# Kernel tuning notes

Hardware: AMD Instinct MI355X
Metric: run time of the kernel (lower is better)

The kernel has to match this reference:

```python
import jax, jax.numpy as jnp
import numpy as np

S = 1024      # graphs (frames / LSTM seq_len)
NPG = 64      # nodes per graph
N = S * NPG   # total nodes
E = 524288    # total edges (512 per graph)
NF, EF = 32, 16
HC = 64       # hidden_channels
H1 = 3        # gat1 heads
NEG_SLOPE = 0.2


def _p(k, shape):
    return 0.1 * jax.random.normal(k, shape, dtype=jnp.float32)


def setup_inputs():
    key = jax.random.key(0)
    ks = jax.random.split(key, 30)
    x = jax.random.normal(ks[0], (N, NF), jnp.float32)
    local = jax.random.randint(ks[1], (2, E), 0, NPG)
    off = jnp.repeat(jnp.arange(S) * NPG, E // S)  # edges grouped per graph
    edge_index = local + off[None, :]
    edge_attr = jax.random.normal(ks[2], (E, EF), jnp.float32)
    batch = jnp.repeat(jnp.arange(S), NPG)
    return {
        'x': x, 'edge_index': edge_index, 'edge_attr': edge_attr, 'batch': batch,
        # gat1: in=NF, out=HC, heads=H1, edge_dim=EF
        'Wl1': _p(ks[3], (NF, H1 * HC)), 'bl1': _p(ks[4], (H1 * HC,)),
        'Wr1': _p(ks[5], (NF, H1 * HC)), 'br1': _p(ks[6], (H1 * HC,)),
        'We1': _p(ks[7], (EF, H1 * HC)), 'att1': _p(ks[8], (H1, HC)),
        'bias1': _p(ks[9], (H1 * HC,)),
        # gat2: in=H1*HC, out=HC, heads=1
        'Wl2': _p(ks[10], (H1 * HC, HC)), 'bl2': _p(ks[11], (HC,)),
        'Wr2': _p(ks[12], (H1 * HC, HC)), 'br2': _p(ks[13], (HC,)),
        'We2': _p(ks[14], (EF, HC)), 'att2': _p(ks[15], (1, HC)),
        'bias2': _p(ks[16], (HC,)),
        # LSTM (torch gate order i,f,g,o)
        'Wih': _p(ks[17], (4 * HC, HC)), 'Whh': _p(ks[18], (4 * HC, HC)),
        'bih': _p(ks[19], (4 * HC,)), 'bhh': _p(ks[20], (4 * HC,)),
        # MLP head
        'W1': _p(ks[21], (HC, HC // 2)), 'b1': _p(ks[22], (HC // 2,)),
        'W2': _p(ks[23], (HC // 2, 1)), 'b2': _p(ks[24], (1,)),
    }


def gatv2(x, edge_index, edge_attr, Wl, bl, Wr, br, We, att, bias, H, C):
    n = x.shape[0]
    src, dst = edge_index[0], edge_index[1]
    # add self loops, edge_attr filled with per-target mean (PyG fill_value='mean')
    deg = jax.ops.segment_sum(jnp.ones((edge_attr.shape[0],), x.dtype), dst, num_segments=n)
    loop_attr = jax.ops.segment_sum(edge_attr, dst, num_segments=n) / jnp.maximum(deg, 1.0)[:, None]
    ar = jnp.arange(n)
    src_f = jnp.concatenate([src, ar])
    dst_f = jnp.concatenate([dst, ar])
    ea_f = jnp.concatenate([edge_attr, loop_attr], axis=0)
    xl = (x @ Wl + bl).reshape(n, H, C)   # source-side transform (message carrier)
    xr = (x @ Wr + br).reshape(n, H, C)   # target-side transform
    eproj = (ea_f @ We).reshape(-1, H, C)
    m = jax.nn.leaky_relu(xl[src_f] + xr[dst_f] + eproj, NEG_SLOPE)  # [Ef,H,C]
    score = jnp.einsum('ehc,hc->eh', m, att)
    smax = jax.ops.segment_max(score, dst_f, num_segments=n)
    expv = jnp.exp(score - smax[dst_f])
    denom = jax.ops.segment_sum(expv, dst_f, num_segments=n)
    alpha = expv / (denom[dst_f] + 1e-16)
    out = jax.ops.segment_sum(alpha[..., None] * xl[src_f], dst_f, num_segments=n)
    return out.reshape(n, H * C) + bias


def lstm_last_hidden(seq, Wih, Whh, bih, bhh):
    # seq: [S, HC]; torch LSTM single layer, h0=c0=0
    def step(carry, xt):
        h, c = carry
        g = Wih @ xt + Whh @ h + bih + bhh
        i, f, gg, o = jnp.split(g, 4)
        c = jax.nn.sigmoid(f) * c + jax.nn.sigmoid(i) * jnp.tanh(gg)
        h = jax.nn.sigmoid(o) * jnp.tanh(c)
        return (h, c), None
    (h, c), _ = jax.lax.scan(step, (jnp.zeros((HC,), seq.dtype), jnp.zeros((HC,), seq.dtype)), seq)
    return h


def reference(x, edge_index, edge_attr, batch, Wl1, bl1, Wr1, br1, We1, att1, bias1,
              Wl2, bl2, Wr2, br2, We2, att2, bias2, Wih, Whh, bih, bhh, W1, b1, W2, b2):
    h = jax.nn.elu(gatv2(x, edge_index, edge_attr, Wl1, bl1, Wr1, br1, We1, att1, bias1, H1, HC))
    h = jax.nn.elu(gatv2(h, edge_index, edge_attr, Wl2, bl2, Wr2, br2, We2, att2, bias2, 1, HC))
    cnt = jax.ops.segment_sum(jnp.ones((N, 1), h.dtype), batch, num_segments=S)
    pooled = jax.ops.segment_sum(h, batch, num_segments=S) / cnt  # [S, HC]
    last = lstm_last_hidden(pooled, Wih, Whh, bih, bhh)[None, :]  # [1, HC]; dropout is identity in eval
    out = jax.nn.relu(last @ W1 + b1) @ W2 + b2  # [1, 1]
    return out
```

## Files before the change

kernel.cpp:

```cpp
#include <hip/hip_runtime.h>

#define ETOT 524288
#define SGR  1024
#define NPG  64
#define EPG  512
#define NFD  32
#define EFD  16
#define HCD  64
#define H1S  196

typedef float f2v __attribute__((ext_vector_type(2)));

__device__ __forceinline__ float elu_(float x){ return x>0.f ? x : (__expf(x)-1.f); }
__device__ __forceinline__ float sig_(float x){ return 1.f/(1.f+__expf(-x)); }
__device__ __forceinline__ float tanhf_(float x){ float e=__expf(2.f*x); return 1.f-2.f/(e+1.f); }
__device__ __forceinline__ float lrelu_(float x){ return x>0.f ? x : 0.2f*x; }

template<int C>
__device__ __forceinline__ float dppf(float v){
  return __int_as_float(__builtin_amdgcn_update_dpp(0, __float_as_int(v), C, 0xF, 0xF, true));
}
__device__ __forceinline__ float quad_add(float v){
  v += dppf<0xB1>(v);
  return v + dppf<0x4E>(v);
}

__device__ void build_csr_la(int tid, int g, const int* ei, const float* ea,
                             int* s_edge, int* s_entry, int* s_off, int* s_deg,
                             int* s_cnt, float* s_la)
{
  const int base = g*NPG;
  const int* srcp = ei + (size_t)g*EPG;
  const int* dstp = ei + (size_t)ETOT + (size_t)g*EPG;
  s_edge[tid] = (srcp[tid]-base) | ((dstp[tid]-base)<<6);
  __syncthreads();
  { const int d=tid>>3, s=tid&7, b0=s*64;
    int c=0;
    #pragma unroll 8
    for(int i=0;i<64;i++) c += (((s_edge[b0+i]>>6)&63)==d);
    s_cnt[(d<<3)|s]=c; }
  __syncthreads();
  if(tid<64){ int a=0;
    #pragma unroll
    for(int s=0;s<8;s++) a+=s_cnt[(tid<<3)|s];
    s_deg[tid]=a; }
  __syncthreads();
  if(tid==0){ int a=0;
    for(int i=0;i<64;i++){ s_off[i]=a; a+=s_deg[i]; }
    s_off[64]=a; }
  __syncthreads();
  { const int d=tid>>3, s=tid&7, b0=s*64;
    int pos=s_off[d];
    for(int s2=0;s2<s;s2++) pos += s_cnt[(d<<3)|s2];
    for(int i=0;i<64;i++){ int en=s_edge[b0+i];
      if(((en>>6)&63)==d) s_entry[pos++] = (en&63) | (d<<6) | ((b0+i)<<12); } }
  __syncthreads();
  if(tid<256){ int n=tid>>2, f0=(tid&3)*4;
    float a0=0,a1=0,a2=0,a3=0;
    const int b=s_off[n], en=s_off[n+1];
    for(int p=b;p<en;p++){ int eid=s_entry[p]>>12;
      const float4 v = *(const float4*)(ea + ((size_t)g*EPG+(size_t)eid)*EFD + f0);
      a0+=v.x; a1+=v.y; a2+=v.z; a3+=v.w; }
    float inv = 1.f/fmaxf((float)(en-b),1.f);
    float4 r; r.x=a0*inv; r.y=a1*inv; r.z=a2*inv; r.w=a3*inv;
    *(float4*)(s_la + n*EFD + f0) = r; }
  __syncthreads();
}

__device__ void scores_softmax(int tid, int g, const float* ea,
   const int* s_entry, const int* s_off, const float* s_la,
   const float* s_We, const float* s_att, const float* s_xl, const float* s_xr,
   float* s_sc)
{
  for(int p=tid;p<576;p+=512){
    int src,dst; float eav[16];
    if(p<EPG){
      int en=s_entry[p]; src=en&63; dst=(en>>6)&63; int eid=en>>12;
      const float* epp = ea + ((size_t)g*EPG + (size_t)eid)*EFD;
      float4 v0=*(const float4*)(epp),   v1=*(const float4*)(epp+4);
      float4 v2=*(const float4*)(epp+8), v3=*(const float4*)(epp+12);
      eav[0]=v0.x;eav[1]=v0.y;eav[2]=v0.z;eav[3]=v0.w;
      eav[4]=v1.x;eav[5]=v1.y;eav[6]=v1.z;eav[7]=v1.w;
      eav[8]=v2.x;eav[9]=v2.y;eav[10]=v2.z;eav[11]=v2.w;
      eav[12]=v3.x;eav[13]=v3.y;eav[14]=v3.z;eav[15]=v3.w;
    } else {
      int n=p-EPG; src=n; dst=n;
      const float* epp = s_la + n*EFD;
      float4 v0=*(const float4*)(epp),   v1=*(const float4*)(epp+4);
      float4 v2=*(const float4*)(epp+8), v3=*(const float4*)(epp+12);
      eav[0]=v0.x;eav[1]=v0.y;eav[2]=v0.z;eav[3]=v0.w;
      eav[4]=v1.x;eav[5]=v1.y;eav[6]=v1.z;eav[7]=v1.w;
      eav[8]=v2.x;eav[9]=v2.y;eav[10]=v2.z;eav[11]=v2.w;
      eav[12]=v3.x;eav[13]=v3.y;eav[14]=v3.z;eav[15]=v3.w;
    }
    float score=0.f;
    #pragma unroll 4
    for(int cq=0;cq<16;cq++){
      float e0=0.f,e1=0.f,e2=0.f,e3=0.f;
      #pragma unroll
      for(int f=0;f<16;f++){
        const float4 wv=*(const float4*)(s_We + f*64 + cq*4);
        e0+=eav[f]*wv.x; e1+=eav[f]*wv.y; e2+=eav[f]*wv.z; e3+=eav[f]*wv.w;
      }
      const float4 xlv=*(const float4*)(s_xl + src*64 + ((cq^(src&15))<<2));
      const float4 xrv=*(const float4*)(s_xr + dst*64 + ((cq^(dst&15))<<2));
      const float4 av =*(const float4*)(s_att + cq*4);
      float m0=lrelu_(xlv.x+xrv.x+e0), m1=lrelu_(xlv.y+xrv.y+e1);
      float m2=lrelu_(xlv.z+xrv.z+e2), m3=lrelu_(xlv.w+xrv.w+e3);
      score += m0*av.x+m1*av.y+m2*av.z+m3*av.w;
    }
    s_sc[p]=score;
  }
  __syncthreads();
  { const int d=tid>>3, s=tid&7;
    const int b=s_off[d], e=s_off[d+1];
    float mx=-1e30f;
    for(int p=b+s;p<e;p+=8) mx=fmaxf(mx,s_sc[p]);
    if(s==0) mx=fmaxf(mx,s_sc[EPG+d]);
    mx=fmaxf(mx,dppf<0xB1>(mx));
    mx=fmaxf(mx,dppf<0x4E>(mx));
    mx=fmaxf(mx,dppf<0x141>(mx));
    float den=0.f;
    for(int p=b+s;p<e;p+=8){ float w=__expf(s_sc[p]-mx); s_sc[p]=w; den+=w; }
    float selfv=0.f;
    if(s==0){ selfv=__expf(s_sc[EPG+d]-mx); den+=selfv; }
    den+=dppf<0xB1>(den);
    den+=dppf<0x4E>(den);
    den+=dppf<0x141>(den);
    const float inv=1.f/(den+1e-16f);
    for(int p=b+s;p<e;p+=8) s_sc[p]*=inv;
    if(s==0) s_sc[EPG+d]=selfv*inv;
  }
  __syncthreads();
}

__device__ __forceinline__ float dot2_(f2v w0,f2v w1,f2v w2,f2v w3,f2v w4,f2v w5,f2v w6,f2v w7,
                                       f2v h0,f2v h1,f2v h2,f2v h3,f2v h4,f2v h5,f2v h6,f2v h7){
  f2v a = w0*h0; a += w1*h1; a += w2*h2; a += w3*h3;
  f2v b = w4*h4; b += w5*h5; b += w6*h6; b += w7*h7;
  f2v s = a+b; return s[0]+s[1];
}

#define WDECL(m) \
  f2v w##m##_0,w##m##_1,w##m##_2,w##m##_3,w##m##_4,w##m##_5,w##m##_6,w##m##_7; \
  { const float* wp_ = Whh + (size_t)((m)*64+l)*64 + q*16; \
    const float4 a_=*(const float4*)(wp_),   b_=*(const float4*)(wp_+4); \
    const float4 c_=*(const float4*)(wp_+8), d_=*(const float4*)(wp_+12); \
    w##m##_0=(f2v){a_.x,a_.y}; w##m##_1=(f2v){a_.z,a_.w}; \
    w##m##_2=(f2v){b_.x,b_.y}; w##m##_3=(f2v){b_.z,b_.w}; \
    w##m##_4=(f2v){c_.x,c_.y}; w##m##_5=(f2v){c_.z,c_.w}; \
    w##m##_6=(f2v){d_.x,d_.y}; w##m##_7=(f2v){d_.z,d_.w}; } \
  asm volatile("" : "+v"(w##m##_0),"+v"(w##m##_1),"+v"(w##m##_2),"+v"(w##m##_3), \
                    "+v"(w##m##_4),"+v"(w##m##_5),"+v"(w##m##_6),"+v"(w##m##_7));

#define DOTP(m) dot2_(w##m##_0,w##m##_1,w##m##_2,w##m##_3,w##m##_4,w##m##_5,w##m##_6,w##m##_7, \
                      hb0,hb1,hb2,hb3,hb4,hb5,hb6,hb7)

#define XQDECL(k) \
  float xq##k##_0,xq##k##_1,xq##k##_2,xq##k##_3; \
  { const float* xpp_ = xproj + (size_t)(k)*256; \
    xq##k##_0=xpp_[l]; xq##k##_1=xpp_[64+l]; xq##k##_2=xpp_[128+l]; xq##k##_3=xpp_[192+l]; }

#define STEP(k) { \
    f2v hb0,hb1,hb2,hb3,hb4,hb5,hb6,hb7; \
    { const float* hp_ = &s_h[cur][q*16]; \
      const float4 a_=*(const float4*)(hp_),   b_=*(const float4*)(hp_+4); \
      const float4 c_=*(const float4*)(hp_+8), d_=*(const float4*)(hp_+12); \
      hb0=(f2v){a_.x,a_.y}; hb1=(f2v){a_.z,a_.w}; \
      hb2=(f2v){b_.x,b_.y}; hb3=(f2v){b_.z,b_.w}; \
      hb4=(f2v){c_.x,c_.y}; hb5=(f2v){c_.z,c_.w}; \
      hb6=(f2v){d_.x,d_.y}; hb7=(f2v){d_.z,d_.w}; } \
    const float cx0=xq##k##_0, cx1=xq##k##_1, cx2=xq##k##_2, cx3=xq##k##_3; \
    if(tb+(k)+4<1024){ \
      const float* xpp_ = xproj + (size_t)(tb+(k)+4)*256; \
      xq##k##_0=xpp_[l]; xq##k##_1=xpp_[64+l]; xq##k##_2=xpp_[128+l]; xq##k##_3=xpp_[192+l]; \
    } \
    float a0=quad_add(DOTP(0)); \
    float a1=quad_add(DOTP(1)); \
    float a2=quad_add(DOTP(2)); \
    float a3=quad_add(DOTP(3)); \
    const float gi=a0+cx0, gf=a1+cx1, gg=a2+cx2, go=a3+cx3; \
    c = sig_(gf)*c + sig_(gi)*tanhf_(gg); \
    const float hn = sig_(go)*tanhf_(c); \
    if(q==0 && tid<256) s_h[cur^1][l]=hn; \
    cur^=1; \
    __syncthreads(); \
  }

__global__ __attribute__((amdgpu_flat_work_group_size(512,512), amdgpu_waves_per_eu(2,2)))
void fused_k(
    const float* __restrict__ x, const int* __restrict__ ei, const float* __restrict__ ea,
    const float* __restrict__ Wl1, const float* __restrict__ bl1,
    const float* __restrict__ Wr1, const float* __restrict__ br1,
    const float* __restrict__ We1, const float* __restrict__ att1, const float* __restrict__ bias1,
    const float* __restrict__ Wl2, const float* __restrict__ bl2,
    const float* __restrict__ Wr2, const float* __restrict__ br2,
    const float* __restrict__ We2, const float* __restrict__ att2, const float* __restrict__ bias2,
    const float* __restrict__ Wih, const float* __restrict__ bih, const float* __restrict__ bhh,
    const float* __restrict__ Whh,
    const float* __restrict__ W1, const float* __restrict__ b1,
    const float* __restrict__ W2, const float* __restrict__ b2,
    float* __restrict__ xproj, int* __restrict__ flags, float* __restrict__ out)
{
  __shared__ __align__(16) float s_x[NPG*36];
  __shared__ __align__(16) float s_h1[NPG*H1S];
  __shared__ __align__(16) float s_xl[NPG*64];
  __shared__ __align__(16) float s_xr[NPG*64];
  __shared__ __align__(16) float s_W[2*32*64];
  __shared__ __align__(16) float s_We[16*64];
  __shared__ __align__(16) float s_att[64];
  __shared__ __align__(16) float s_la[NPG*EFD];
  __shared__ float s_sc[576];
  __shared__ float s_pool[64];
  __shared__ int   s_edge[EPG];
  __shared__ int   s_entry[EPG];
  __shared__ int   s_cnt[512];
  __shared__ int   s_off[65];
  __shared__ int   s_deg[64];
  __shared__ __align__(16) float s_h[2][64];
  __shared__ float s_y[32];
  __shared__ int   s_rd;

  const int tid = threadIdx.x;

  if(blockIdx.x == 0){
    const int l=(tid>>2)&63, q=tid&3;
    WDECL(0) WDECL(1) WDECL(2) WDECL(3)
    float c=0.f;
    if(tid<64){ s_h[0][tid]=0.f; s_h[1][tid]=0.f; }
    if(tid==0) s_rd = -1;
    __syncthreads();
    if(tid==0){ int r=s_rd;
      while(r<3){ while(__hip_atomic_load(&flags[r+1], __ATOMIC_ACQUIRE, __HIP_MEMORY_SCOPE_AGENT)==0){ __builtin_amdgcn_s_sleep(2); } r++; }
      s_rd=r; }
    __syncthreads();
    XQDECL(0) XQDECL(1) XQDECL(2) XQDECL(3)
    int cur=0;
    for(int tb=0;tb<1024;tb+=4){
      const int need = (tb+7<1023)?(tb+7):1023;
      if(tid==0){ int r=s_rd;
        while(r<need){ while(__hip_atomic_load(&flags[r+1], __ATOMIC_ACQUIRE, __HIP_MEMORY_SCOPE_AGENT)==0){ __builtin_amdgcn_s_sleep(2); } r++; }
        s_rd=r; }
      __syncthreads();
      STEP(0) STEP(1) STEP(2) STEP(3)
    }
    if(tid<32){
      float a=b1[tid];
      #pragma unroll 8
      for(int k=0;k<64;k++) a += s_h[cur][k]*W1[k*32+tid];
      s_y[tid]=fmaxf(a,0.f);
    }
    __syncthreads();
    if(tid==0){
      float a=b2[0];
      #pragma unroll
      for(int j=0;j<32;j++) a += s_y[j]*W2[j];
      out[0]=a;
    }
    return;
  }

  const int g = blockIdx.x - 1;
  const int base = g*NPG;

  { int n=tid>>3, kq=tid&7;
    float4 v = *(const float4*)(x + (size_t)(base+n)*NFD + kq*4);
    *(float4*)(s_x + n*36 + kq*4) = v; }

  build_csr_la(tid, g, ei, ea, s_edge, s_entry, s_off, s_deg, s_cnt, s_la);

  for(int h=0;h<3;h++){
    { int k=tid>>4, c0=(tid&15)*4;
      *(float4*)(s_W + k*64 + c0)        = *(const float4*)(Wl1 + (size_t)k*192 + h*64 + c0);
      *(float4*)(s_W + 2048 + k*64 + c0) = *(const float4*)(Wr1 + (size_t)k*192 + h*64 + c0); }
    if(tid<256){ int f=tid>>4, c0=(tid&15)*4;
      *(float4*)(s_We + f*64 + c0) = *(const float4*)(We1 + (size_t)f*192 + h*64 + c0); }
    if(tid<16) *(float4*)(s_att + tid*4) = *(const float4*)(att1 + h*64 + tid*4);
    __syncthreads();

    { const int cg=tid&15, ng=tid>>4, n0=ng*2, c0=cg*4;
      const float4 blv=*(const float4*)(bl1 + h*64 + c0);
      const float4 brv=*(const float4*)(br1 + h*64 + c0);
      float accl[2][4]={{blv.x,blv.y,blv.z,blv.w},{blv.x,blv.y,blv.z,blv.w}};
      float accr[2][4]={{brv.x,brv.y,brv.z,brv.w},{brv.x,brv.y,brv.z,brv.w}};
      #pragma unroll
      for(int kq=0;kq<8;kq++){
        float xs0[4], xs1[4];
        { float4 v=*(const float4*)(s_x + n0*36 + kq*4);     xs0[0]=v.x;xs0[1]=v.y;xs0[2]=v.z;xs0[3]=v.w; }
        { float4 v=*(const float4*)(s_x + (n0+1)*36 + kq*4); xs1[0]=v.x;xs1[1]=v.y;xs1[2]=v.z;xs1[3]=v.w; }
        #pragma unroll
        for(int f=0;f<4;f++){
          const float4 wl=*(const float4*)(s_W + (kq*4+f)*64 + c0);
          const float4 wr=*(const float4*)(s_W + 2048 + (kq*4+f)*64 + c0);
          accl[0][0]+=xs0[f]*wl.x; accl[0][1]+=xs0[f]*wl.y; accl[0][2]+=xs0[f]*wl.z; accl[0][3]+=xs0[f]*wl.w;
          accl[1][0]+=xs1[f]*wl.x; accl[1][1]+=xs1[f]*wl.y; accl[1][2]+=xs1[f]*wl.z; accl[1][3]+=xs1[f]*wl.w;
          accr[0][0]+=xs0[f]*wr.x; accr[0][1]+=xs0[f]*wr.y; accr[0][2]+=xs0[f]*wr.z; accr[0][3]+=xs0[f]*wr.w;
          accr[1][0]+=xs1[f]*wr.x; accr[1][1]+=xs1[f]*wr.y; accr[1][2]+=xs1[f]*wr.z; accr[1][3]+=xs1[f]*wr.w;
        }
      }
      #pragma unroll
      for(int i=0;i<2;i++){
        const int n=n0+i, sq=((cg^(n&15))<<2);
        float4 vl; vl.x=accl[i][0]; vl.y=accl[i][1]; vl.z=accl[i][2]; vl.w=accl[i][3];
        float4 vr; vr.x=accr[i][0]; vr.y=accr[i][1]; vr.z=accr[i][2]; vr.w=accr[i][3];
        *(float4*)(s_xl + n*64 + sq)=vl;
        *(float4*)(s_xr + n*64 + sq)=vr;
      }
    }
    __syncthreads();

    scores_softmax(tid, g, ea, s_entry, s_off, s_la, s_We, s_att, s_xl, s_xr, s_sc);

    { const int n=tid>>3, c0a=(tid&7)*8;
      float acc[8]={0.f,0.f,0.f,0.f,0.f,0.f,0.f,0.f};
      const int b=s_off[n], e=s_off[n+1];
      for(int p=b;p<e;p++){
        const int en=s_entry[p], src=en&63;
        const float a=s_sc[p];
        #pragma unroll
        for(int qq=0;qq<2;qq++){
          const int cq=(c0a>>2)+qq;
          const float4 xv=*(const float4*)(s_xl + src*64 + ((cq^(src&15))<<2));
          acc[qq*4+0]+=a*xv.x; acc[qq*4+1]+=a*xv.y; acc[qq*4+2]+=a*xv.z; acc[qq*4+3]+=a*xv.w;
        }
      }
      { const float a=s_sc[EPG+n];
        #pragma unroll
        for(int qq=0;qq<2;qq++){
          const int cq=(c0a>>2)+qq;
          const float4 xv=*(const float4*)(s_xl + n*64 + ((cq^(n&15))<<2));
          acc[qq*4+0]+=a*xv.x; acc[qq*4+1]+=a*xv.y; acc[qq*4+2]+=a*xv.z; acc[qq*4+3]+=a*xv.w;
        } }
      #pragma unroll
      for(int qq=0;qq<2;qq++){
        const float4 bv=*(const float4*)(bias1 + h*64 + c0a + qq*4);
        float4 r; r.x=elu_(acc[qq*4+0]+bv.x); r.y=elu_(acc[qq*4+1]+bv.y);
                  r.z=elu_(acc[qq*4+2]+bv.z); r.w=elu_(acc[qq*4+3]+bv.w);
        *(float4*)(s_h1 + n*H1S + h*64 + c0a + qq*4)=r;
      }
    }
    __syncthreads();
  }

  const int cg=tid&15, ng=tid>>4, n0=ng*2, gc0=cg*4;
  float accl[2][4], accr[2][4];
  { const float4 blv=*(const float4*)(bl2 + gc0);
    const float4 brv=*(const float4*)(br2 + gc0);
    #pragma unroll
    for(int i=0;i<2;i++){
      accl[i][0]=blv.x; accl[i][1]=blv.y; accl[i][2]=blv.z; accl[i][3]=blv.w;
      accr[i][0]=brv.x; accr[i][1]=brv.y; accr[i][2]=brv.z; accr[i][3]=brv.w; } }
  for(int kc=0;kc<6;kc++){
    { int k=tid>>4, cc=(tid&15)*4;
      *(float4*)(s_W + k*64 + cc)        = *(const float4*)(Wl2 + (size_t)(kc*32+k)*64 + cc);
      *(float4*)(s_W + 2048 + k*64 + cc) = *(const float4*)(Wr2 + (size_t)(kc*32+k)*64 + cc); }
    __syncthreads();
    #pragma unroll
    for(int kq=0;kq<8;kq++){
      float xs0[4], xs1[4];
      { float4 v=*(const float4*)(s_h1 + n0*H1S + kc*32 + kq*4);     xs0[0]=v.x;xs0[1]=v.y;xs0[2]=v.z;xs0[3]=v.w; }
      { float4 v=*(const float4*)(s_h1 + (n0+1)*H1S + kc*32 + kq*4); xs1[0]=v.x;xs1[1]=v.y;xs1[2]=v.z;xs1[3]=v.w; }
      #pragma unroll
      for(int f=0;f<4;f++){
        const float4 wl=*(const float4*)(s_W + (kq*4+f)*64 + gc0);
        const float4 wr=*(const float4*)(s_W + 2048 + (kq*4+f)*64 + gc0);
        accl[0][0]+=xs0[f]*wl.x; accl[0][1]+=xs0[f]*wl.y; accl[0][2]+=xs0[f]*wl.z; accl[0][3]+=xs0[f]*wl.w;
        accl[1][0]+=xs1[f]*wl.x; accl[1][1]+=xs1[f]*wl.y; accl[1][2]+=xs1[f]*wl.z; accl[1][3]+=xs1[f]*wl.w;
        accr[0][0]+=xs0[f]*wr.x; accr[0][1]+=xs0[f]*wr.y; accr[0][2]+=xs0[f]*wr.z; accr[0][3]+=xs0[f]*wr.w;
        accr[1][0]+=xs1[f]*wr.x; accr[1][1]+=xs1[f]*wr.y; accr[1][2]+=xs1[f]*wr.z; accr[1][3]+=xs1[f]*wr.w;
      }
    }
    __syncthreads();
  }
  #pragma unroll
  for(int i=0;i<2;i++){
    const int n=n0+i, sq=((cg^(n&15))<<2);
    float4 vl; vl.x=accl[i][0]; vl.y=accl[i][1]; vl.z=accl[i][2]; vl.w=accl[i][3];
    float4 vr; vr.x=accr[i][0]; vr.y=accr[i][1]; vr.z=accr[i][2]; vr.w=accr[i][3];
    *(float4*)(s_xl + n*64 + sq)=vl;
    *(float4*)(s_xr + n*64 + sq)=vr;
  }
  if(tid<256){ int f=tid>>4, cc=(tid&15)*4;
    *(float4*)(s_We + f*64 + cc) = *(const float4*)(We2 + (size_t)f*64 + cc); }
  if(tid<16) *(float4*)(s_att + tid*4) = *(const float4*)(att2 + tid*4);
  __syncthreads();

  scores_softmax(tid, g, ea, s_entry, s_off, s_la, s_We, s_att, s_xl, s_xr, s_sc);

  float* s_out = s_W;
  { const int n=tid>>3, c0a=(tid&7)*8;
    float acc[8]={0.f,0.f,0.f,0.f,0.f,0.f,0.f,0.f};
    const int b=s_off[n], e=s_off[n+1];
    for(int p=b;p<e;p++){
      const int en=s_entry[p], src=en&63;
      const float a=s_sc[p];
      #pragma unroll
      for(int qq=0;qq<2;qq++){
        const int cq=(c0a>>2)+qq;
        const float4 xv=*(const float4*)(s_xl + src*64 + ((cq^(src&15))<<2));
        acc[qq*4+0]+=a*xv.x; acc[qq*4+1]+=a*xv.y; acc[qq*4+2]+=a*xv.z; acc[qq*4+3]+=a*xv.w;
      }
    }
    { const float a=s_sc[EPG+n];
      #pragma unroll
      for(int qq=0;qq<2;qq++){
        const int cq=(c0a>>2)+qq;
        const float4 xv=*(const float4*)(s_xl + n*64 + ((cq^(n&15))<<2));
        acc[qq*4+0]+=a*xv.x; acc[qq*4+1]+=a*xv.y; acc[qq*4+2]+=a*xv.z; acc[qq*4+3]+=a*xv.w;
      } }
    #pragma unroll
    for(int qq=0;qq<2;qq++){
      const float4 bv=*(const float4*)(bias2 + c0a + qq*4);
      float4 r; r.x=elu_(acc[qq*4+0]+bv.x); r.y=elu_(acc[qq*4+1]+bv.y);
                r.z=elu_(acc[qq*4+2]+bv.z); r.w=elu_(acc[qq*4+3]+bv.w);
      *(float4*)(s_out + n*64 + c0a + qq*4)=r;
    }
  }
  __syncthreads();
  if(tid<64){ float s=0.f;
    #pragma unroll 8
    for(int n2=0;n2<64;n2++) s += s_out[n2*64+tid];
    s_pool[tid]=s*(1.f/64.f); }
  __syncthreads();
  if(tid<256){
    float a=bih[tid]+bhh[tid];
    #pragma unroll
    for(int kq=0;kq<16;kq++){
      const float4 w=*(const float4*)(Wih + (size_t)tid*64 + kq*4);
      a += w.x*s_pool[kq*4+0] + w.y*s_pool[kq*4+1] + w.z*s_pool[kq*4+2] + w.w*s_pool[kq*4+3];
    }
    xproj[(size_t)g*256 + tid]=a;
  }
  __syncthreads();
  if(tid==0){
    __threadfence();
    __hip_atomic_store(&flags[g], 1, __ATOMIC_RELEASE, __HIP_MEMORY_SCOPE_AGENT);
  }
}

extern "C" void kernel_launch(void* const* d_in, const int* in_sizes, int n_in,
                              void* d_out, int out_size, void* d_ws, size_t ws_size,
                              hipStream_t stream) {
  (void)in_sizes; (void)n_in; (void)out_size; (void)ws_size;
  const float* x    = (const float*)d_in[0];
  const int*   ei   = (const int*)d_in[1];
  const float* ea   = (const float*)d_in[2];
  const float* Wl1  = (const float*)d_in[4];
  const float* bl1  = (const float*)d_in[5];
  const float* Wr1  = (const float*)d_in[6];
  const float* br1  = (const float*)d_in[7];
  const float* We1  = (const float*)d_in[8];
  const float* att1 = (const float*)d_in[9];
  const float* bias1= (const float*)d_in[10];
  const float* Wl2  = (const float*)d_in[11];
  const float* bl2  = (const float*)d_in[12];
  const float* Wr2  = (const float*)d_in[13];
  const float* br2  = (const float*)d_in[14];
  const float* We2  = (const float*)d_in[15];
  const float* att2 = (const float*)d_in[16];
  const float* bias2= (const float*)d_in[17];
  const float* Wih  = (const float*)d_in[18];
  const float* Whh  = (const float*)d_in[19];
  const float* bih  = (const float*)d_in[20];
  const float* bhh  = (const float*)d_in[21];
  const float* W1   = (const float*)d_in[22];
  const float* b1   = (const float*)d_in[23];
  const float* W2   = (const float*)d_in[24];
  const float* b2   = (const float*)d_in[25];

  float* xpw   = (float*)d_ws;
  int*   flags = (int*)((char*)d_ws + (size_t)1048576);
  float* outp  = (float*)d_out;

  hipMemsetAsync(flags, 0, 1024*sizeof(int), stream);
  fused_k<<<dim3(SGR+1), dim3(512), 0, stream>>>(
      x, ei, ea, Wl1, bl1, Wr1, br1, We1, att1, bias1,
      Wl2, bl2, Wr2, br2, We2, att2, bias2,
      Wih, bih, bhh, Whh, W1, b1, W2, b2,
      xpw, flags, outp);
}
```

Before: 823.2 us.

## Spill GAT layer-1 output to global workspace to shrink LDS and raise occupancy

The per-block shared buffer holding the layer-1 GAT output (64x196 floats) is removed. That output is now written to a global workspace and re-staged in 32-column chunks through the existing s_x buffer during the layer-2 projection. This cuts LDS use per block, and the waves_per_eu hint is relaxed from (2,2) to (1,4) so more blocks can be co-resident. The LSTM block also drops its 4-deep register prefetch of the input projections for a 1-step lookahead, which lowers register pressure but exposes more global load latency on the sequential critical path. The trade is extra global write and read traffic for the hidden features.

```diff
diff --git a/kernel.cpp b/kernel.cpp
--- a/kernel.cpp
+++ b/kernel.cpp
@@ -7,7 +7,6 @@
 #define NFD  32
 #define EFD  16
 #define HCD  64
-#define H1S  196
 
 typedef float f2v __attribute__((ext_vector_type(2)));
 
@@ -156,12 +155,7 @@
 #define DOTP(m) dot2_(w##m##_0,w##m##_1,w##m##_2,w##m##_3,w##m##_4,w##m##_5,w##m##_6,w##m##_7, \
                       hb0,hb1,hb2,hb3,hb4,hb5,hb6,hb7)
 
-#define XQDECL(k) \
-  float xq##k##_0,xq##k##_1,xq##k##_2,xq##k##_3; \
-  { const float* xpp_ = xproj + (size_t)(k)*256; \
-    xq##k##_0=xpp_[l]; xq##k##_1=xpp_[64+l]; xq##k##_2=xpp_[128+l]; xq##k##_3=xpp_[192+l]; }
-
-#define STEP(k) { \
+#define STEP(T) { \
     f2v hb0,hb1,hb2,hb3,hb4,hb5,hb6,hb7; \
     { const float* hp_ = &s_h[cur][q*16]; \
       const float4 a_=*(const float4*)(hp_),   b_=*(const float4*)(hp_+4); \
@@ -170,24 +164,25 @@
       hb2=(f2v){b_.x,b_.y}; hb3=(f2v){b_.z,b_.w}; \
       hb4=(f2v){c_.x,c_.y}; hb5=(f2v){c_.z,c_.w}; \
       hb6=(f2v){d_.x,d_.y}; hb7=(f2v){d_.z,d_.w}; } \
-    const float cx0=xq##k##_0, cx1=xq##k##_1, cx2=xq##k##_2, cx3=xq##k##_3; \
-    if(tb+(k)+4<1024){ \
-      const float* xpp_ = xproj + (size_t)(tb+(k)+4)*256; \
-      xq##k##_0=xpp_[l]; xq##k##_1=xpp_[64+l]; xq##k##_2=xpp_[128+l]; xq##k##_3=xpp_[192+l]; \
+    float xn0=0.f,xn1=0.f,xn2=0.f,xn3=0.f; \
+    if((T)<1023){ \
+      const float* xpp_ = xproj + (size_t)((T)+1)*256; \
+      xn0=xpp_[l]; xn1=xpp_[64+l]; xn2=xpp_[128+l]; xn3=xpp_[192+l]; \
     } \
     float a0=quad_add(DOTP(0)); \
     float a1=quad_add(DOTP(1)); \
     float a2=quad_add(DOTP(2)); \
     float a3=quad_add(DOTP(3)); \
-    const float gi=a0+cx0, gf=a1+cx1, gg=a2+cx2, go=a3+cx3; \
+    const float gi=a0+xp0, gf=a1+xp1, gg=a2+xp2, go=a3+xp3; \
     c = sig_(gf)*c + sig_(gi)*tanhf_(gg); \
     const float hn = sig_(go)*tanhf_(c); \
     if(q==0 && tid<256) s_h[cur^1][l]=hn; \
+    xp0=xn0; xp1=xn1; xp2=xn2; xp3=xn3; \
     cur^=1; \
     __syncthreads(); \
   }
 
-__global__ __attribute__((amdgpu_flat_work_group_size(512,512), amdgpu_waves_per_eu(2,2)))
+__global__ __attribute__((amdgpu_flat_work_group_size(512,512), amdgpu_waves_per_eu(1,4)))
 void fused_k(
     const float* __restrict__ x, const int* __restrict__ ei, const float* __restrict__ ea,
     const float* __restrict__ Wl1, const float* __restrict__ bl1,
@@ -200,10 +195,10 @@
     const float* __restrict__ Whh,
     const float* __restrict__ W1, const float* __restrict__ b1,
     const float* __restrict__ W2, const float* __restrict__ b2,
-    float* __restrict__ xproj, int* __restrict__ flags, float* __restrict__ out)
+    float* __restrict__ h1w, float* __restrict__ xproj, int* __restrict__ flags,
+    float* __restrict__ out)
 {
   __shared__ __align__(16) float s_x[NPG*36];
-  __shared__ __align__(16) float s_h1[NPG*H1S];
   __shared__ __align__(16) float s_xl[NPG*64];
   __shared__ __align__(16) float s_xr[NPG*64];
   __shared__ __align__(16) float s_W[2*32*64];
@@ -234,7 +229,7 @@
       while(r<3){ while(__hip_atomic_load(&flags[r+1], __ATOMIC_ACQUIRE, __HIP_MEMORY_SCOPE_AGENT)==0){ __builtin_amdgcn_s_sleep(2); } r++; }
       s_rd=r; }
     __syncthreads();
-    XQDECL(0) XQDECL(1) XQDECL(2) XQDECL(3)
+    float xp0=xproj[l], xp1=xproj[64+l], xp2=xproj[128+l], xp3=xproj[192+l];
     int cur=0;
     for(int tb=0;tb<1024;tb+=4){
       const int need = (tb+7<1023)?(tb+7):1023;
@@ -242,7 +237,7 @@
         while(r<need){ while(__hip_atomic_load(&flags[r+1], __ATOMIC_ACQUIRE, __HIP_MEMORY_SCOPE_AGENT)==0){ __builtin_amdgcn_s_sleep(2); } r++; }
         s_rd=r; }
       __syncthreads();
-      STEP(0) STEP(1) STEP(2) STEP(3)
+      STEP(tb+0) STEP(tb+1) STEP(tb+2) STEP(tb+3)
     }
     if(tid<32){
       float a=b1[tid];
@@ -331,16 +326,19 @@
           const float4 xv=*(const float4*)(s_xl + n*64 + ((cq^(n&15))<<2));
           acc[qq*4+0]+=a*xv.x; acc[qq*4+1]+=a*xv.y; acc[qq*4+2]+=a*xv.z; acc[qq*4+3]+=a*xv.w;
         } }
+      float* op = h1w + (size_t)(base+n)*192 + h*64 + c0a;
       #pragma unroll
       for(int qq=0;qq<2;qq++){
         const float4 bv=*(const float4*)(bias1 + h*64 + c0a + qq*4);
         float4 r; r.x=elu_(acc[qq*4+0]+bv.x); r.y=elu_(acc[qq*4+1]+bv.y);
                   r.z=elu_(acc[qq*4+2]+bv.z); r.w=elu_(acc[qq*4+3]+bv.w);
-        *(float4*)(s_h1 + n*H1S + h*64 + c0a + qq*4)=r;
-      }
-    }
-    __syncthreads();
-  }
+        *(float4*)(op + qq*4)=r;
+      }
+    }
+    __syncthreads();
+  }
+  __threadfence_block();
+  __syncthreads();
 
   const int cg=tid&15, ng=tid>>4, n0=ng*2, gc0=cg*4;
   float accl[2][4], accr[2][4];
@@ -351,6 +349,8 @@
       accl[i][0]=blv.x; accl[i][1]=blv.y; accl[i][2]=blv.z; accl[i][3]=blv.w;
       accr[i][0]=brv.x; accr[i][1]=brv.y; accr[i][2]=brv.z; accr[i][3]=brv.w; } }
   for(int kc=0;kc<6;kc++){
+    { int n=tid>>3, kq=tid&7;
+      *(float4*)(s_x + n*36 + kq*4) = *(const float4*)(h1w + (size_t)(base+n)*192 + kc*32 + kq*4); }
     { int k=tid>>4, cc=(tid&15)*4;
       *(float4*)(s_W + k*64 + cc)        = *(const float4*)(Wl2 + (size_t)(kc*32+k)*64 + cc);
       *(float4*)(s_W + 2048 + k*64 + cc) = *(const float4*)(Wr2 + (size_t)(kc*32+k)*64 + cc); }
@@ -358,8 +358,8 @@
     #pragma unroll
     for(int kq=0;kq<8;kq++){
       float xs0[4], xs1[4];
-      { float4 v=*(const float4*)(s_h1 + n0*H1S + kc*32 + kq*4);     xs0[0]=v.x;xs0[1]=v.y;xs0[2]=v.z;xs0[3]=v.w; }
-      { float4 v=*(const float4*)(s_h1 + (n0+1)*H1S + kc*32 + kq*4); xs1[0]=v.x;xs1[1]=v.y;xs1[2]=v.z;xs1[3]=v.w; }
+      { float4 v=*(const float4*)(s_x + n0*36 + kq*4);     xs0[0]=v.x;xs0[1]=v.y;xs0[2]=v.z;xs0[3]=v.w; }
+      { float4 v=*(const float4*)(s_x + (n0+1)*36 + kq*4); xs1[0]=v.x;xs1[1]=v.y;xs1[2]=v.z;xs1[3]=v.w; }
       #pragma unroll
       for(int f=0;f<4;f++){
         const float4 wl=*(const float4*)(s_W + (kq*4+f)*64 + gc0);
@@ -468,8 +468,9 @@
   const float* W2   = (const float*)d_in[24];
   const float* b2   = (const float*)d_in[25];
 
-  float* xpw   = (float*)d_ws;
-  int*   flags = (int*)((char*)d_ws + (size_t)1048576);
+  float* h1w   = (float*)d_ws;
+  float* xpw   = (float*)((char*)d_ws + (size_t)50331648);
+  int*   flags = (int*)((char*)d_ws + (size_t)51380224);
   float* outp  = (float*)d_out;
 
   hipMemsetAsync(flags, 0, 1024*sizeof(int), stream);
@@ -477,5 +478,5 @@
       x, ei, ea, Wl1, bl1, Wr1, br1, We1, att1, bias1,
       Wl2, bl2, Wr2, br2, We2, att2, bias2,
       Wih, bih, bhh, Whh, W1, b1, W2, b2,
-      xpw, flags, outp);
-}
+      h1w, xpw, flags, outp);
+}
```

Result: slower. 853.5 us (+3.7%).
